# Kernel optimization log

Measured on AMD Instinct MI355X. Metric: run time of the kernel, lower is better.

The kernel has to match this reference:

```python
import jax, jax.numpy as jnp
import numpy as np

ALPHA = 0.1
MARGIN = 1.0
SLOPE = 0.2  # LeakyReLU negative_slope
OFFSET = 1.0e6

def leaky(x):
    return jnp.where(x >= 0, x, SLOPE * x)

def _xavier(key, shape, gain=np.sqrt(2.0)):
    fan_out, fan_in = shape[0], shape[1]
    std = gain * np.sqrt(2.0 / (fan_in + fan_out))
    return jax.random.normal(key, shape, dtype=jnp.float32) * std

def setup_inputs() -> dict:
    key = jax.random.key(0)
    ks = jax.random.split(key, 8)
    B, F, T, D, H = 32768, 128, 32, 16, 10
    return {
        "X": jax.random.normal(ks[0], (B, F), dtype=jnp.float32),
        "affine_weights": jax.random.normal(ks[1], (T, F, D), dtype=jnp.float32),
        "W0": _xavier(ks[2], (H, D)),
        "W1": _xavier(ks[3], (H, H)),
        "W2": _xavier(ks[4], (H, H)),
        "W3": _xavier(ks[5], (H, H)),
        "Wh": _xavier(ks[6], (T, H)),
        "bh": jnp.zeros((T,), dtype=jnp.float32),
    }

def reference(X, affine_weights, W0, W1, W2, W3, Wh, bh):
    T = affine_weights.shape[0]
    # goad_transforms: x_trans [B, trans_dim, n_trans]; labels[b,t] = t (implicit)
    x_trans = jnp.einsum('bn,ant->bta', X, affine_weights)
    # ConvNet encoder, kernel_size=1 convs == per-position channel matmuls
    h = jnp.einsum('od,bdt->bot', W0, x_trans)
    for W in (W1, W2, W3):
        h = jnp.einsum('od,bdt->bot', W, leaky(h))
    rep = h                                   # [B, H, T]
    # head: LeakyReLU + Conv1d(H->T, bias=True)
    pred = jnp.einsum('oh,bht->bot', Wh, leaky(rep)) + bh[None, :, None]  # [B, T, T]
    batch_rep = jnp.transpose(rep, (0, 2, 1))  # [B, T, H]
    # CrossEntropy(reduction='none') with labels[b,t]=t -> -diag of log_softmax over class dim
    logp = jax.nn.log_softmax(pred, axis=1)
    loss_ce = -jnp.diagonal(logp, axis1=1, axis2=2)          # [B, T]
    # triplet center loss
    means = jnp.mean(batch_rep, axis=0)                       # [T, H]
    res = jnp.sum((batch_rep[:, :, None, :] - means[None, None, :, :]) ** 2, axis=-1)  # [B,T,T]
    pos = jnp.diagonal(res, axis1=1, axis2=2)                 # [B, T]
    neg = jnp.min(res + jnp.eye(T, dtype=res.dtype) * OFFSET, axis=-1)  # [B, T]
    loss_tc = jnp.mean(jnp.maximum(pos + MARGIN - neg, 0.0))  # scalar
    loss = jnp.mean(ALPHA * loss_tc + loss_ce, axis=1)        # [B]
    return batch_rep, loss
```

## Files before the change

kernel.cpp:

```cpp
#include <hip/hip_runtime.h>

typedef __attribute__((ext_vector_type(8))) short bf16x8;
typedef __attribute__((ext_vector_type(4))) float f32x4;

#define BTOT 32768
#define FDIM 128
#define TDIM 32
#define DDIM 16
#define HDIM 10
#define CDIM 320
#define ALPHA_C 0.1f
#define MARGIN_C 1.0f
#define SLOPE_C 0.2f
#define OFFSET_C 1.0e6f

#define WS_A0P  0
#define WS_MEAN 32768
#define WS_TC   33088
#define WS_CE   33152

__device__ __forceinline__ float leaky(float x) { return fmaxf(x, SLOPE_C * x); }

__device__ __forceinline__ unsigned short f2bf(float f) {
    unsigned int u = __float_as_uint(f);
    u += 0x7fffu + ((u >> 16) & 1u);
    return (unsigned short)(u >> 16);
}

__device__ __forceinline__ f32x4 mfma32(bf16x8 a, bf16x8 b, f32x4 c) {
    return __builtin_amdgcn_mfma_f32_16x16x32_bf16(a, b, c, 0, 0, 0);
}

__device__ __forceinline__ void leaky_pack(f32x4 v, unsigned& p0, unsigned& p1) {
    float a0 = leaky(v[0]), a1 = leaky(v[1]), a2 = leaky(v[2]), a3 = leaky(v[3]);
    asm("v_cvt_pk_bf16_f32 %0, %1, %2" : "=v"(p0) : "v"(a0), "v"(a1));
    asm("v_cvt_pk_bf16_f32 %0, %1, %2" : "=v"(p1) : "v"(a2), "v"(a3));
}

__device__ __forceinline__ bf16x8 build_bfrag(unsigned p0, unsigned p1, int g, int r16) {
    int s0 = ((2 * g) * 16 + r16) & 63;
    int s1 = ((2 * g + 1) * 16 + r16) & 63;
    unsigned w0 = (unsigned)__shfl((int)p0, s0, 64);
    unsigned w1 = (unsigned)__shfl((int)p1, s0, 64);
    unsigned w2 = (unsigned)__shfl((int)p0, s1, 64);
    unsigned w3 = (unsigned)__shfl((int)p1, s1, 64);
    unsigned zm = (g < 2) ? 0xFFFFFFFFu : 0u;
    union { unsigned u[4]; bf16x8 v; } r;
    r.u[0] = w0 & zm; r.u[1] = w1 & zm; r.u[2] = w2 & zm; r.u[3] = w3 & zm;
    return r.v;
}

__global__ void prep_kernel(const float* __restrict__ aw, const float* __restrict__ W0,
                            unsigned short* __restrict__ a0p) {
    int idx = blockIdx.x * blockDim.x + threadIdx.x;
    if (idx >= 65536) return;
    int n = idx & 127, o = (idx >> 7) & 15, t = idx >> 11;
    unsigned short r = 0;
    if (o < 10) {
        const float* a = aw + ((size_t)t * FDIM + n) * DDIM;
        const float* w = W0 + o * DDIM;
        float s = 0.f;
#pragma unroll
        for (int d = 0; d < DDIM; ++d) s += a[d] * w[d];
        r = f2bf(s);
    }
    a0p[idx] = r;
}

__global__ __launch_bounds__(256, 4) void gemm0_fused(
    const float* __restrict__ X, const unsigned short* __restrict__ a0p,
    const float* __restrict__ W1, const float* __restrict__ W2,
    const float* __restrict__ W3, const float* __restrict__ Wh,
    const float* __restrict__ bh,
    float* __restrict__ rep, float* __restrict__ ce_acc,
    float* __restrict__ mean_acc)
{
    __shared__ unsigned short xs[32][136];
    __shared__ unsigned short w1x[16][32], w2x[16][32], w3x[16][32], whx[32][32];
    __shared__ float mred[2][32][12];

    int tid = threadIdx.x;
    int b0 = blockIdx.x * 32;

#pragma unroll
    for (int k = 0; k < 4; ++k) {
        int idx = tid + k * 256;
        int row = idx >> 5, col4 = idx & 31;
        float4 v = reinterpret_cast<const float4*>(X + (size_t)(b0 + row) * FDIM)[col4];
        unsigned p0, p1;
        asm("v_cvt_pk_bf16_f32 %0, %1, %2" : "=v"(p0) : "v"(v.x), "v"(v.y));
        asm("v_cvt_pk_bf16_f32 %0, %1, %2" : "=v"(p1) : "v"(v.z), "v"(v.w));
        uint2 pk; pk.x = p0; pk.y = p1;
        *reinterpret_cast<uint2*>(&xs[row][col4 * 4]) = pk;
    }
#pragma unroll
    for (int k = 0; k < 2; ++k) {
        int i = tid + k * 256;
        int o = i >> 5, kk = i & 31;
        bool in10 = (o < 10 && kk < 10);
        w1x[o][kk] = in10 ? f2bf(W1[o * 10 + kk]) : (unsigned short)0;
        w2x[o][kk] = in10 ? f2bf(W2[o * 10 + kk]) : (unsigned short)0;
        w3x[o][kk] = in10 ? f2bf(W3[o * 10 + kk]) : (unsigned short)0;
    }
#pragma unroll
    for (int k = 0; k < 4; ++k) {
        int i = tid + k * 256;
        int o = i >> 5, kk = i & 31;
        whx[o][kk] = (kk < 10) ? f2bf(Wh[o * 10 + kk]) : (unsigned short)0;
    }
    __syncthreads();

    int lane = tid & 63, w = __builtin_amdgcn_readfirstlane(tid >> 6);
    int r16 = lane & 15, g = lane >> 4;
    int bsub = w >> 1, thalf = w & 1;
    int bglob = b0 + bsub * 16 + r16;

    bf16x8 xf[4];
#pragma unroll
    for (int s = 0; s < 4; ++s)
        xf[s] = *reinterpret_cast<const bf16x8*>(&xs[bsub * 16 + r16][s * 32 + g * 8]);

    bf16x8 w1f = *reinterpret_cast<const bf16x8*>(&w1x[r16][g * 8]);
    bf16x8 w2f = *reinterpret_cast<const bf16x8*>(&w2x[r16][g * 8]);
    bf16x8 w3f = *reinterpret_cast<const bf16x8*>(&w3x[r16][g * 8]);
    bf16x8 whAf = *reinterpret_cast<const bf16x8*>(&whx[r16][g * 8]);
    bf16x8 whBf = *reinterpret_cast<const bf16x8*>(&whx[16 + r16][g * 8]);
    f32x4 bhA, bhB;
#pragma unroll
    for (int r = 0; r < 4; ++r) { bhA[r] = bh[g * 4 + r]; bhB[r] = bh[16 + g * 4 + r]; }
    const f32x4 zero4 = {0.f, 0.f, 0.f, 0.f};

    float ce_local = 0.f;

    for (int tt4 = 0; tt4 < 4; ++tt4) {
#pragma unroll
        for (int q = 0; q < 4; ++q) {
            int t = thalf * 16 + tt4 * 4 + q;
            const bf16x8* ap = reinterpret_cast<const bf16x8*>(
                a0p + ((size_t)t * 16 + r16) * 128);
            f32x4 acc = zero4;
#pragma unroll
            for (int s = 0; s < 4; ++s)
                acc = mfma32(ap[s * 4 + g], xf[s], acc);

            unsigned p0, p1;
            leaky_pack(acc, p0, p1);
            bf16x8 bf = build_bfrag(p0, p1, g, r16);
            f32x4 d1 = mfma32(w1f, bf, zero4);
            leaky_pack(d1, p0, p1);
            bf = build_bfrag(p0, p1, g, r16);
            f32x4 d2 = mfma32(w2f, bf, zero4);
            leaky_pack(d2, p0, p1);
            bf = build_bfrag(p0, p1, g, r16);
            f32x4 d3 = mfma32(w3f, bf, zero4);

            float* rp = rep + (size_t)bglob * CDIM + t * HDIM + g * 4;
            if (g < 2) {
                float2 v0; v0.x = d3[0]; v0.y = d3[1];
                float2 v1; v1.x = d3[2]; v1.y = d3[3];
                reinterpret_cast<float2*>(rp)[0] = v0;
                reinterpret_cast<float2*>(rp)[1] = v1;
            } else if (g == 2) {
                float2 v0; v0.x = d3[0]; v0.y = d3[1];
                reinterpret_cast<float2*>(rp)[0] = v0;
            }

            float m0 = d3[0], m1 = d3[1], m2 = d3[2], m3 = d3[3];
#pragma unroll
            for (int msk = 1; msk < 16; msk <<= 1) {
                m0 += __shfl_xor(m0, msk, 64);
                m1 += __shfl_xor(m1, msk, 64);
                m2 += __shfl_xor(m2, msk, 64);
                m3 += __shfl_xor(m3, msk, 64);
            }
            if (r16 == 0 && g < 3) {
                float4 mv; mv.x = m0; mv.y = m1; mv.z = m2; mv.w = m3;
                *reinterpret_cast<float4*>(&mred[bsub][t][g * 4]) = mv;
            }

            leaky_pack(d3, p0, p1);
            bf = build_bfrag(p0, p1, g, r16);
            f32x4 pA = mfma32(whAf, bf, bhA);
            f32x4 pB = mfma32(whBf, bf, bhB);

            float mx = fmaxf(fmaxf(fmaxf(pA[0], pA[1]), fmaxf(pA[2], pA[3])),
                             fmaxf(fmaxf(pB[0], pB[1]), fmaxf(pB[2], pB[3])));
            mx = fmaxf(mx, __shfl_xor(mx, 16, 64));
            mx = fmaxf(mx, __shfl_xor(mx, 32, 64));
            float se = __expf(pA[0] - mx) + __expf(pA[1] - mx) +
                       __expf(pA[2] - mx) + __expf(pA[3] - mx) +
                       __expf(pB[0] - mx) + __expf(pB[1] - mx) +
                       __expf(pB[2] - mx) + __expf(pB[3] - mx);
            se += __shfl_xor(se, 16, 64);
            se += __shfl_xor(se, 32, 64);
            float lse = mx + __logf(se);
            float pr = thalf ? pB[q] : pA[q];
            float ptv = __shfl(pr, tt4 * 16 + r16, 64);
            ce_local += lse - ptv;
        }
    }

    if (g == 0) atomicAdd(&ce_acc[bglob], ce_local);
    __syncthreads();
    for (int i = tid; i < TDIM * HDIM; i += 256) {
        int t = i / 10, o = i - t * 10;
        atomicAdd(&mean_acc[i], mred[0][t][o] + mred[1][t][o]);
    }
}

__global__ __launch_bounds__(256) void tc_kernel(const float* __restrict__ rep,
    const float* __restrict__ mean_acc, float* __restrict__ tc_sum)
{
    __shared__ float tile[32][CDIM];
    __shared__ float mm[CDIM];
    __shared__ float msq[TDIM];
    __shared__ float wpart[4];
    int tid = threadIdx.x;
    int b0 = blockIdx.x * 32;

    for (int i = tid; i < CDIM; i += 256) mm[i] = mean_acc[i] * (1.f / BTOT);
    const float4* src = reinterpret_cast<const float4*>(rep + (size_t)b0 * CDIM);
#pragma unroll
    for (int k = 0; k < 10; ++k) {
        int idx = tid + k * 256;
        int row = idx / 80, col4 = idx - row * 80;
        *reinterpret_cast<float4*>(&tile[row][col4 * 4]) = src[idx];
    }
    __syncthreads();
    if (tid < TDIM) {
        float s = 0.f;
#pragma unroll
        for (int h = 0; h < HDIM; ++h) { float v = mm[tid * HDIM + h]; s += v * v; }
        msq[tid] = s;
    }
    __syncthreads();

    int t = tid & 31, bg = tid >> 5;
    float rv[4][HDIM], rsq[4];
#pragma unroll
    for (int j = 0; j < 4; ++j) {
        const float* rp = &tile[bg * 4 + j][t * HDIM];
        float s = 0.f;
#pragma unroll
        for (int q = 0; q < 5; ++q) {
            float2 v = reinterpret_cast<const float2*>(rp)[q];
            rv[j][2 * q] = v.x; rv[j][2 * q + 1] = v.y;
            s += v.x * v.x + v.y * v.y;
        }
        rsq[j] = s;
    }
    float pos[4], neg[4];
#pragma unroll
    for (int j = 0; j < 4; ++j) { pos[j] = 0.f; neg[j] = 1e30f; }
#pragma unroll 4
    for (int c = 0; c < TDIM; ++c) {
        float m0[HDIM];
#pragma unroll
        for (int q = 0; q < 5; ++q) {
            float2 v = reinterpret_cast<const float2*>(&mm[c * HDIM])[q];
            m0[2 * q] = v.x; m0[2 * q + 1] = v.y;
        }
        float mq = msq[c];
        bool isT = (c == t);
#pragma unroll
        for (int j = 0; j < 4; ++j) {
            float dot = 0.f;
#pragma unroll
            for (int h = 0; h < HDIM; ++h) dot += rv[j][h] * m0[h];
            float s = rsq[j] - 2.f * dot + mq;
            if (isT) pos[j] = s;
            float s2 = isT ? s + OFFSET_C : s;
            neg[j] = fminf(neg[j], s2);
        }
    }
    float hs = 0.f;
#pragma unroll
    for (int j = 0; j < 4; ++j) hs += fmaxf(pos[j] + MARGIN_C - neg[j], 0.f);
#pragma unroll
    for (int m = 1; m < 64; m <<= 1) hs += __shfl_xor(hs, m, 64);
    int lane = tid & 63, w = tid >> 6;
    if (lane == 0) wpart[w] = hs;
    __syncthreads();
    if (tid == 0) atomicAdd(tc_sum, wpart[0] + wpart[1] + wpart[2] + wpart[3]);
}

__global__ void final_kernel(const float* __restrict__ ce_acc,
                             const float* __restrict__ tc_sum, float* __restrict__ loss)
{
    int b = blockIdx.x * blockDim.x + threadIdx.x;
    if (b < BTOT)
        loss[b] = ALPHA_C * (tc_sum[0] * (1.f / ((float)BTOT * TDIM)))
                + ce_acc[b] * (1.f / TDIM);
}

extern "C" void kernel_launch(void* const* d_in, const int* in_sizes, int n_in,
                              void* d_out, int out_size, void* d_ws, size_t ws_size,
                              hipStream_t stream) {
    const float* X  = (const float*)d_in[0];
    const float* aw = (const float*)d_in[1];
    const float* W0 = (const float*)d_in[2];
    const float* W1 = (const float*)d_in[3];
    const float* W2 = (const float*)d_in[4];
    const float* W3 = (const float*)d_in[5];
    const float* Wh = (const float*)d_in[6];
    const float* bh = (const float*)d_in[7];
    float* ws = (float*)d_ws;
    unsigned short* a0p = (unsigned short*)(ws + WS_A0P);
    float* mean_acc = ws + WS_MEAN;
    float* tc_sum   = ws + WS_TC;
    float* ce_acc   = ws + WS_CE;
    float* out_rep = (float*)d_out;
    float* loss = out_rep + (size_t)BTOT * TDIM * HDIM;

    hipMemsetAsync(mean_acc, 0, (384 + BTOT) * sizeof(float), stream);
    prep_kernel<<<256, 256, 0, stream>>>(aw, W0, a0p);
    gemm0_fused<<<BTOT / 32, 256, 0, stream>>>(X, a0p, W1, W2, W3, Wh, bh,
                                               out_rep, ce_acc, mean_acc);
    tc_kernel<<<BTOT / 32, 256, 0, stream>>>(out_rep, mean_acc, tc_sum);
    final_kernel<<<BTOT / 256, 256, 0, stream>>>(ce_acc, tc_sum, loss);
}
```

Measured before the change: 102.9 us.

## Split gemm0 blocks across T halves and interleave MFMA accumulators

```diff
diff --git a/kernel.cpp b/kernel.cpp
--- a/kernel.cpp
+++ b/kernel.cpp
@@ -67,7 +67,7 @@
     a0p[idx] = r;
 }
 
-__global__ __launch_bounds__(256, 4) void gemm0_fused(
+__global__ __launch_bounds__(256, 8) void gemm0_fused(
     const float* __restrict__ X, const unsigned short* __restrict__ a0p,
     const float* __restrict__ W1, const float* __restrict__ W2,
     const float* __restrict__ W3, const float* __restrict__ Wh,
@@ -77,10 +77,11 @@
 {
     __shared__ unsigned short xs[32][136];
     __shared__ unsigned short w1x[16][32], w2x[16][32], w3x[16][32], whx[32][32];
-    __shared__ float mred[2][32][12];
+    __shared__ float mred[2][16][12];
 
     int tid = threadIdx.x;
-    int b0 = blockIdx.x * 32;
+    int b0 = (blockIdx.x >> 1) * 32;
+    int thalf = blockIdx.x & 1;
 
 #pragma unroll
     for (int k = 0; k < 4; ++k) {
@@ -112,7 +113,7 @@
 
     int lane = tid & 63, w = __builtin_amdgcn_readfirstlane(tid >> 6);
     int r16 = lane & 15, g = lane >> 4;
-    int bsub = w >> 1, thalf = w & 1;
+    int bsub = w >> 1, tq = w & 1;
     int bglob = b0 + bsub * 16 + r16;
 
     bf16x8 xf[4];
@@ -132,16 +133,21 @@
 
     float ce_local = 0.f;
 
-    for (int tt4 = 0; tt4 < 4; ++tt4) {
+    for (int tt2 = 0; tt2 < 2; ++tt2) {
 #pragma unroll
         for (int q = 0; q < 4; ++q) {
-            int t = thalf * 16 + tt4 * 4 + q;
+            int tloc = tq * 8 + tt2 * 4 + q;
+            int t = thalf * 16 + tloc;
             const bf16x8* ap = reinterpret_cast<const bf16x8*>(
                 a0p + ((size_t)t * 16 + r16) * 128);
-            f32x4 acc = zero4;
-#pragma unroll
-            for (int s = 0; s < 4; ++s)
-                acc = mfma32(ap[s * 4 + g], xf[s], acc);
+            f32x4 accA = zero4, accB = zero4;
+            accA = mfma32(ap[0 * 4 + g], xf[0], accA);
+            accB = mfma32(ap[1 * 4 + g], xf[1], accB);
+            accA = mfma32(ap[2 * 4 + g], xf[2], accA);
+            accB = mfma32(ap[3 * 4 + g], xf[3], accB);
+            f32x4 acc;
+#pragma unroll
+            for (int r = 0; r < 4; ++r) acc[r] = accA[r] + accB[r];
 
             unsigned p0, p1;
             leaky_pack(acc, p0, p1);
@@ -175,7 +181,7 @@
             }
             if (r16 == 0 && g < 3) {
                 float4 mv; mv.x = m0; mv.y = m1; mv.z = m2; mv.w = m3;
-                *reinterpret_cast<float4*>(&mred[bsub][t][g * 4]) = mv;
+                *reinterpret_cast<float4*>(&mred[bsub][tloc][g * 4]) = mv;
             }
 
             leaky_pack(d3, p0, p1);
@@ -195,16 +201,17 @@
             se += __shfl_xor(se, 32, 64);
             float lse = mx + __logf(se);
             float pr = thalf ? pB[q] : pA[q];
-            float ptv = __shfl(pr, tt4 * 16 + r16, 64);
+            float ptv = __shfl(pr, (tq * 2 + tt2) * 16 + r16, 64);
             ce_local += lse - ptv;
         }
     }
 
     if (g == 0) atomicAdd(&ce_acc[bglob], ce_local);
     __syncthreads();
-    for (int i = tid; i < TDIM * HDIM; i += 256) {
-        int t = i / 10, o = i - t * 10;
-        atomicAdd(&mean_acc[i], mred[0][t][o] + mred[1][t][o]);
+    for (int i = tid; i < 16 * HDIM; i += 256) {
+        int tloc = i / 10, o = i - tloc * 10;
+        atomicAdd(&mean_acc[(thalf * 16 + tloc) * HDIM + o],
+                  mred[0][tloc][o] + mred[1][tloc][o]);
     }
 }
 
@@ -314,8 +321,8 @@
 
     hipMemsetAsync(mean_acc, 0, (384 + BTOT) * sizeof(float), stream);
     prep_kernel<<<256, 256, 0, stream>>>(aw, W0, a0p);
-    gemm0_fused<<<BTOT / 32, 256, 0, stream>>>(X, a0p, W1, W2, W3, Wh, bh,
-                                               out_rep, ce_acc, mean_acc);
+    gemm0_fused<<<2048, 256, 0, stream>>>(X, a0p, W1, W2, W3, Wh, bh,
+                                          out_rep, ce_acc, mean_acc);
     tc_kernel<<<BTOT / 32, 256, 0, stream>>>(out_rep, mean_acc, tc_sum);
     final_kernel<<<BTOT / 256, 256, 0, stream>>>(ce_acc, tc_sum, loss);
 }
```

After: 159.2 us. +54.7%, slower.
